# Kernel optimization log

Measured on AMD Instinct MI355X. Metric: run time of the kernel, lower is better.

Reference implementation:

```python
import jax, jax.numpy as jnp
import numpy as np

B, T, D = 8, 4096, 1024

def setup_inputs() -> dict:
    key = jax.random.key(0)
    ks = jax.random.split(key, 7)
    s1 = 1.0 / np.sqrt(D)
    return {
        "x":  jax.random.normal(ks[0], (B, T, D), dtype=jnp.float32),
        "W1": jax.random.normal(ks[1], (D, D), dtype=jnp.float32) * s1,   # attn_1.weight [out,in]
        "b1": jnp.zeros((D,), dtype=jnp.float32),
        "w2": jax.random.normal(ks[2], (1, D), dtype=jnp.float32) * s1,   # attn_2.weight [1,in]
        "b2": jnp.zeros((1,), dtype=jnp.float32),
        "Wc": jax.random.normal(ks[3], (D, 2 * D), dtype=jnp.float32) * (1.0 / np.sqrt(2 * D)),
        "bc": jnp.zeros((D,), dtype=jnp.float32),
    }

def reference(x, W1, b1, w2, b2, Wc, bc):
    # additive attention scores: [B, T, 1] -> [B, T]
    h = jnp.tanh(jnp.einsum('btd,ed->bte', x, W1) + b1)
    s = (jnp.einsum('btd,od->bto', h, w2) + b2)[..., 0]          # [B, T]
    # causal prefix softmax via cumulative sums (single O(T) pass).
    # softmax is shift-invariant, so subtracting the global per-batch max is stable.
    m = jnp.max(s, axis=1, keepdims=True)                        # [B, 1]
    e = jnp.exp(s - m)                                           # [B, T]
    num = jnp.cumsum(e[..., None] * x, axis=1)                   # [B, T, D]
    den = jnp.cumsum(e, axis=1)[..., None]                       # [B, T, 1]
    ctx = num / den                                              # [B, T, D]
    combined = jnp.concatenate((ctx, x), axis=2)                 # [B, T, 2D]
    out = jnp.tanh(jnp.einsum('btk,dk->btd', combined, Wc) + bc)
    return out
```

## Files before the change

kernel.cpp:

```cpp
#include <hip/hip_runtime.h>
#include <cmath>


#define Mtot 32768
#define Dd 1024
#define Tt 4096
#define Bb 8
#define NCHUNK 64
#define TCH 64

typedef __bf16 bf16x8 __attribute__((ext_vector_type(8)));
typedef float f32x4 __attribute__((ext_vector_type(4)));

__device__ __forceinline__ unsigned short f2bf(float f) {
  unsigned int u = __float_as_uint(f);
  unsigned int r = (u + 0x7FFFu + ((u >> 16) & 1u)) >> 16;
  return (unsigned short)r;
}
__device__ __forceinline__ float bf2f(unsigned short s) {
  return __uint_as_float(((unsigned int)s) << 16);
}
__device__ __forceinline__ float tanh_fast(float x) {
  return 1.0f - __fdividef(2.0f, __expf(2.0f * x) + 1.0f);
}

__device__ __forceinline__ void gload16(const unsigned short* g, unsigned short* l) {
  __builtin_amdgcn_global_load_lds(
      (const __attribute__((address_space(1))) unsigned int*)g,
      (__attribute__((address_space(3))) unsigned int*)l, 16, 0, 0);
}

__device__ __forceinline__ void mfma_core256(
    const unsigned short* __restrict__ A0, const unsigned short* __restrict__ A1,
    const unsigned short* __restrict__ W, int ldw, int Ktot,
    int m0, int n0, unsigned short* lds, f32x4 acc[8][4]) {
  const int tid = threadIdx.x;
  const int lane = tid & 63, w = tid >> 6;
  const int wm = w >> 2, wn = w & 3;
  const int quad = lane >> 4, c = lane & 15;
  const int lrow = lane >> 3;
  const int col8 = (lane & 7) ^ lrow;
  const int NK = Ktot >> 6;

#define STG(dst, kt_) do {                                                        \
    int k0_ = (kt_) << 6;                                                         \
    const unsigned short* Asrc_ = (k0_ < 1024) ? A0 : A1;                         \
    int ka_ = k0_ & 1023;                                                         \
    _Pragma("unroll")                                                             \
    for (int j = 0; j < 4; ++j) {                                                 \
      int rb_ = j * 64 + w * 8;                                                   \
      gload16(Asrc_ + (size_t)(m0 + rb_ + lrow) * 1024 + ka_ + col8 * 8,          \
              (dst) + rb_ * 64);                                                  \
      gload16(W + (size_t)(n0 + rb_ + lrow) * ldw + k0_ + col8 * 8,               \
              (dst) + 16384 + rb_ * 64);                                          \
    }                                                                             \
  } while (0)

  STG(lds, 0);

#pragma unroll 1
  for (int kt = 0; kt < NK; ++kt) {
    unsigned short* cur = lds + (kt & 1) * 32768;
    unsigned short* nxt = lds + ((kt + 1) & 1) * 32768;
    if (kt + 1 < NK) {
      STG(nxt, kt + 1);
      asm volatile("s_waitcnt vmcnt(8)" ::: "memory");
    } else {
      asm volatile("s_waitcnt vmcnt(0)" ::: "memory");
    }
    __builtin_amdgcn_s_barrier();
    asm volatile("" ::: "memory");

    const unsigned short* As = cur;
    const unsigned short* Bs = cur + 16384;
    bf16x8 bfr[4];
#pragma unroll
    for (int p = 0; p < 4; ++p) {
      const int ks = p >> 1, mh = p & 1;
      if (mh == 0) {
#pragma unroll
        for (int jn = 0; jn < 4; ++jn) {
          int rb = wn * 64 + jn * 16 + c;
          int pb = (ks * 4 + quad) ^ (rb & 7);
          bfr[jn] = *(const bf16x8*)(Bs + rb * 64 + pb * 8);
        }
      }
      bf16x8 af[4];
#pragma unroll
      for (int ii = 0; ii < 4; ++ii) {
        int ra = wm * 128 + (mh * 4 + ii) * 16 + c;
        int pa = (ks * 4 + quad) ^ (ra & 7);
        af[ii] = *(const bf16x8*)(As + ra * 64 + pa * 8);
      }
      asm volatile("" ::: "memory");
      __builtin_amdgcn_s_barrier();
      asm volatile("s_waitcnt lgkmcnt(0)" ::: "memory");
      __builtin_amdgcn_sched_barrier(0);
      __builtin_amdgcn_s_setprio(1);
#pragma unroll
      for (int ii = 0; ii < 4; ++ii)
#pragma unroll
        for (int jn = 0; jn < 4; ++jn)
          acc[mh * 4 + ii][jn] = __builtin_amdgcn_mfma_f32_16x16x32_bf16(
              af[ii], bfr[jn], acc[mh * 4 + ii][jn], 0, 0, 0);
      __builtin_amdgcn_s_setprio(0);
      asm volatile("" ::: "memory");
      __builtin_amdgcn_s_barrier();
      asm volatile("" ::: "memory");
    }
  }
#undef STG
}

__global__ __launch_bounds__(512, 2) void gemm_s(
    const unsigned short* __restrict__ xb, const unsigned short* __restrict__ W1b,
    const float* __restrict__ b1, const float* __restrict__ w2, float* __restrict__ s) {
  __shared__ __align__(16) unsigned short lds[65536];
  f32x4 acc[8][4];
#pragma unroll
  for (int i = 0; i < 8; ++i)
#pragma unroll
    for (int j = 0; j < 4; ++j) acc[i][j] = (f32x4){0.f, 0.f, 0.f, 0.f};
  int bid = blockIdx.x;
  int swz = (bid & 7) * 64 + (bid >> 3);
  int m0 = (swz >> 2) * 256, n0 = (swz & 3) * 256;
  mfma_core256(xb, xb, W1b, 1024, 1024, m0, n0, lds, acc);
  int tid = threadIdx.x, lane = tid & 63, w = tid >> 6;
  int wm = w >> 2, wn = w & 3, quad = lane >> 4, c = lane & 15;
  float w2v[4], b1v[4];
#pragma unroll
  for (int jn = 0; jn < 4; ++jn) {
    int n = n0 + wn * 64 + jn * 16 + c;
    w2v[jn] = w2[n];
    b1v[jn] = b1[n];
  }
#pragma unroll
  for (int i = 0; i < 8; ++i) {
#pragma unroll
    for (int r = 0; r < 4; ++r) {
      float p = 0.f;
#pragma unroll
      for (int jn = 0; jn < 4; ++jn) p += w2v[jn] * tanh_fast(acc[i][jn][r] + b1v[jn]);
      p += __shfl_xor(p, 1, 64);
      p += __shfl_xor(p, 2, 64);
      p += __shfl_xor(p, 4, 64);
      p += __shfl_xor(p, 8, 64);
      if (c == 0) atomicAdd(&s[m0 + wm * 128 + i * 16 + quad * 4 + r], p);
    }
  }
}

__global__ __launch_bounds__(512, 2) void gemm_out(
    const unsigned short* __restrict__ qb, const unsigned short* __restrict__ xb,
    const unsigned short* __restrict__ Wcb, const float* __restrict__ bc_,
    float* __restrict__ out) {
  __shared__ __align__(16) unsigned short lds[65536];
  f32x4 acc[8][4];
#pragma unroll
  for (int i = 0; i < 8; ++i)
#pragma unroll
    for (int j = 0; j < 4; ++j) acc[i][j] = (f32x4){0.f, 0.f, 0.f, 0.f};
  int bid = blockIdx.x;
  int swz = (bid & 7) * 64 + (bid >> 3);
  int m0 = (swz >> 2) * 256, n0 = (swz & 3) * 256;
  mfma_core256(qb, xb, Wcb, 2048, 2048, m0, n0, lds, acc);
  int tid = threadIdx.x, lane = tid & 63, w = tid >> 6;
  int wm = w >> 2, wn = w & 3, quad = lane >> 4, c = lane & 15;
#pragma unroll
  for (int jn = 0; jn < 4; ++jn) {
    int n = n0 + wn * 64 + jn * 16 + c;
    float bias = bc_[n];
#pragma unroll
    for (int i = 0; i < 8; ++i) {
#pragma unroll
      for (int r = 0; r < 4; ++r) {
        int m = m0 + wm * 128 + i * 16 + quad * 4 + r;
        out[(size_t)m * Dd + n] = tanh_fast(acc[i][jn][r] + bias);
      }
    }
  }
}

__global__ __launch_bounds__(256) void cast_all(
    const float4* __restrict__ x, const float4* __restrict__ W1,
    const float4* __restrict__ Wc, ushort4* __restrict__ xb,
    ushort4* __restrict__ W1b, ushort4* __restrict__ Wcb,
    float4* __restrict__ s) {
  int i = blockIdx.x * 256 + threadIdx.x;
  if (i < 8388608) {
    float4 v = x[i];
    ushort4 o;
    o.x = f2bf(v.x); o.y = f2bf(v.y); o.z = f2bf(v.z); o.w = f2bf(v.w);
    xb[i] = o;
  } else if (i < 8650752) {
    int p = i - 8388608;
    float4 v = W1[p];
    ushort4 o;
    o.x = f2bf(v.x); o.y = f2bf(v.y); o.z = f2bf(v.z); o.w = f2bf(v.w);
    W1b[p] = o;
  } else if (i < 9175040) {
    int p = i - 8650752;
    float4 v = Wc[p];
    ushort4 o;
    o.x = f2bf(v.x); o.y = f2bf(v.y); o.z = f2bf(v.z); o.w = f2bf(v.w);
    Wcb[p] = o;
  } else {
    s[i - 9175040] = (float4){0.f, 0.f, 0.f, 0.f};
  }
}

__global__ __launch_bounds__(256) void softmax_scan(
    const float* __restrict__ s, float* __restrict__ e, float* __restrict__ den) {
  int b = blockIdx.x, tid = threadIdx.x;
  int lane = tid & 63, wid = tid >> 6;
  __shared__ float redm[4], wsum[4];
  const float4* sb4 = (const float4*)(s + (size_t)b * Tt);
  float v[16];
#pragma unroll
  for (int j = 0; j < 4; ++j) {
    float4 f = sb4[tid * 4 + j];
    v[j * 4 + 0] = f.x; v[j * 4 + 1] = f.y; v[j * 4 + 2] = f.z; v[j * 4 + 3] = f.w;
  }
  float m = v[0];
#pragma unroll
  for (int j = 1; j < 16; ++j) m = fmaxf(m, v[j]);
#pragma unroll
  for (int off = 32; off > 0; off >>= 1) m = fmaxf(m, __shfl_xor(m, off, 64));
  if (lane == 0) redm[wid] = m;
  __syncthreads();
  m = fmaxf(fmaxf(redm[0], redm[1]), fmaxf(redm[2], redm[3]));
  float ev[16];
  float ls = 0.f;
#pragma unroll
  for (int j = 0; j < 16; ++j) { ev[j] = __expf(v[j] - m); ls += ev[j]; }
  float sc = ls;
#pragma unroll
  for (int off = 1; off < 64; off <<= 1) {
    float tt = __shfl_up(sc, off, 64);
    if (lane >= off) sc += tt;
  }
  if (lane == 63) wsum[wid] = sc;
  __syncthreads();
  float woff = 0.f;
#pragma unroll
  for (int w = 0; w < 4; ++w) woff += (w < wid) ? wsum[w] : 0.f;
  float run = sc - ls + woff;
  float4* eb4 = (float4*)(e + (size_t)b * Tt);
  float4* db4 = (float4*)(den + (size_t)b * Tt);
#pragma unroll
  for (int j = 0; j < 4; ++j) {
    float4 eo, doo;
    run += ev[j * 4 + 0]; eo.x = ev[j * 4 + 0]; doo.x = run;
    run += ev[j * 4 + 1]; eo.y = ev[j * 4 + 1]; doo.y = run;
    run += ev[j * 4 + 2]; eo.z = ev[j * 4 + 2]; doo.z = run;
    run += ev[j * 4 + 3]; eo.w = ev[j * 4 + 3]; doo.w = run;
    eb4[tid * 4 + j] = eo;
    db4[tid * 4 + j] = doo;
  }
}

__global__ __launch_bounds__(1024) void chunk_sums(
    const unsigned short* __restrict__ xb, const float* __restrict__ e,
    float* __restrict__ S) {
  int bc = blockIdx.x;
  int b = bc >> 6, c = bc & 63;
  int d = threadIdx.x;
  const unsigned short* xp = xb + ((size_t)(b * Tt + c * TCH)) * Dd + d;
  const float* eb = e + (size_t)b * Tt + c * TCH;
  float acc = 0.f;
#pragma unroll 8
  for (int t = 0; t < TCH; ++t) acc += eb[t] * bf2f(xp[(size_t)t * Dd]);
  S[((size_t)bc) * Dd + d] = acc;
}

__global__ __launch_bounds__(256) void chunk_prefix(float* __restrict__ S) {
  int idx = blockIdx.x * 256 + threadIdx.x;
  int b = idx >> 10, d = idx & 1023;
  float* Sb = S + (size_t)b * NCHUNK * Dd + d;
  float acc = 0.f;
#pragma unroll 8
  for (int c = 0; c < NCHUNK; ++c) {
    float t = Sb[(size_t)c * Dd];
    Sb[(size_t)c * Dd] = acc;
    acc += t;
  }
}

__global__ __launch_bounds__(1024) void scan_q(
    const unsigned short* __restrict__ xb, const float* __restrict__ e,
    const float* __restrict__ den, const float* __restrict__ S,
    unsigned short* __restrict__ qb) {
  int bc = blockIdx.x;
  int b = bc >> 6, c = bc & 63;
  int d = threadIdx.x;
  int tbase = b * Tt + c * TCH;
  float acc = S[((size_t)bc) * Dd + d];
  const unsigned short* xp = xb + (size_t)tbase * Dd + d;
  const float* eb = e + tbase;
  const float* db = den + tbase;
  unsigned short* qp = qb + (size_t)tbase * Dd + d;
#pragma unroll 4
  for (int t = 0; t < TCH; ++t) {
    acc += eb[t] * bf2f(xp[(size_t)t * Dd]);
    qp[(size_t)t * Dd] = f2bf(acc * __fdividef(1.0f, db[t]));
  }
}

extern "C" void kernel_launch(void* const* d_in, const int* in_sizes, int n_in,
                              void* d_out, int out_size, void* d_ws, size_t ws_size,
                              hipStream_t stream) {
  const float* x  = (const float*)d_in[0];
  const float* W1 = (const float*)d_in[1];
  const float* b1 = (const float*)d_in[2];
  const float* w2 = (const float*)d_in[3];
  const float* Wc = (const float*)d_in[5];
  const float* bc = (const float*)d_in[6];
  float* out = (float*)d_out;

  float* ws = (float*)d_ws;
  float* s_buf   = ws;
  float* e_buf   = ws + 32768;
  float* den_buf = ws + 65536;
  float* S_buf   = ws + 98304;
  unsigned short* qb  = (unsigned short*)(ws + 622592);
  unsigned short* xb  = (unsigned short*)(ws + 17399808);
  unsigned short* W1b = (unsigned short*)(ws + 34177024);
  unsigned short* Wcb = (unsigned short*)(ws + 34701312);

  cast_all<<<35872, 256, 0, stream>>>((const float4*)x, (const float4*)W1,
                                      (const float4*)Wc, (ushort4*)xb,
                                      (ushort4*)W1b, (ushort4*)Wcb,
                                      (float4*)s_buf);

  gemm_s<<<512, 512, 0, stream>>>(xb, W1b, b1, w2, s_buf);
  softmax_scan<<<Bb, 256, 0, stream>>>(s_buf, e_buf, den_buf);
  chunk_sums<<<Bb * NCHUNK, 1024, 0, stream>>>(xb, e_buf, S_buf);
  chunk_prefix<<<Bb * Dd / 256, 256, 0, stream>>>(S_buf);
  scan_q<<<Bb * NCHUNK, 1024, 0, stream>>>(xb, e_buf, den_buf, S_buf, qb);
  gemm_out<<<512, 512, 0, stream>>>(qb, xb, Wcb, bc, out);
}
```

Measured before the change: 496.3 us.

## Split GEMM k-tile staging into half-k sub-tiles interleaved with MFMA phases

Reorganizes the LDS layout of each 64-wide k tile into two 32-wide halves with a 4-way XOR swizzle. Global-to-LDS loads for the next tile are spread across the four MFMA phases instead of being issued all at once at the top of the iteration. Finer-grained vmcnt waits let compute on the first half proceed while the second half is still loading. The aim is to hide load latency and drop one barrier per iteration. The cost is more complex wait bookkeeping and a risk of races if the vmcnt counts are wrong.

New measurement: 501.8 us. Within noise of the previous version (+1.1%).

```diff
diff --git a/kernel.cpp b/kernel.cpp
--- a/kernel.cpp
+++ b/kernel.cpp
@@ -38,41 +38,38 @@
   const int lane = tid & 63, w = tid >> 6;
   const int wm = w >> 2, wn = w & 3;
   const int quad = lane >> 4, c = lane & 15;
-  const int lrow = lane >> 3;
-  const int col8 = (lane & 7) ^ lrow;
+  const int lr16 = lane >> 2;
+  const int csw = (lane & 3) ^ (lr16 & 3);
   const int NK = Ktot >> 6;
 
-#define STG(dst, kt_) do {                                                        \
-    int k0_ = (kt_) << 6;                                                         \
+#define STGA(dstbase, kt_, h_) do {                                               \
+    int k0_ = ((kt_) << 6) + (h_) * 32;                                           \
     const unsigned short* Asrc_ = (k0_ < 1024) ? A0 : A1;                         \
     int ka_ = k0_ & 1023;                                                         \
     _Pragma("unroll")                                                             \
-    for (int j = 0; j < 4; ++j) {                                                 \
-      int rb_ = j * 64 + w * 8;                                                   \
-      gload16(Asrc_ + (size_t)(m0 + rb_ + lrow) * 1024 + ka_ + col8 * 8,          \
-              (dst) + rb_ * 64);                                                  \
-      gload16(W + (size_t)(n0 + rb_ + lrow) * ldw + k0_ + col8 * 8,               \
-              (dst) + 16384 + rb_ * 64);                                          \
+    for (int j = 0; j < 2; ++j) {                                                 \
+      gload16(Asrc_ + (size_t)(m0 + j * 128 + w * 16 + lr16) * 1024 + ka_ + csw * 8, \
+              (dstbase) + (h_) * 8192 + (j * 128 + w * 16) * 32);                 \
     }                                                                             \
   } while (0)
-
-  STG(lds, 0);
+#define STGB(dstbase, kt_, h_) do {                                               \
+    int k0_ = ((kt_) << 6) + (h_) * 32;                                           \
+    _Pragma("unroll")                                                             \
+    for (int j = 0; j < 2; ++j) {                                                 \
+      gload16(W + (size_t)(n0 + j * 128 + w * 16 + lr16) * ldw + k0_ + csw * 8,   \
+              (dstbase) + 16384 + (h_) * 8192 + (j * 128 + w * 16) * 32);         \
+    }                                                                             \
+  } while (0)
+
+  STGA(lds, 0, 0); STGB(lds, 0, 0); STGA(lds, 0, 1); STGB(lds, 0, 1);
+  asm volatile("s_waitcnt vmcnt(4)" ::: "memory");
+  __builtin_amdgcn_s_barrier();
 
 #pragma unroll 1
   for (int kt = 0; kt < NK; ++kt) {
     unsigned short* cur = lds + (kt & 1) * 32768;
     unsigned short* nxt = lds + ((kt + 1) & 1) * 32768;
-    if (kt + 1 < NK) {
-      STG(nxt, kt + 1);
-      asm volatile("s_waitcnt vmcnt(8)" ::: "memory");
-    } else {
-      asm volatile("s_waitcnt vmcnt(0)" ::: "memory");
-    }
-    __builtin_amdgcn_s_barrier();
-    asm volatile("" ::: "memory");
-
-    const unsigned short* As = cur;
-    const unsigned short* Bs = cur + 16384;
+    const bool more = (kt + 1 < NK);
     bf16x8 bfr[4];
 #pragma unroll
     for (int p = 0; p < 4; ++p) {
@@ -81,16 +78,25 @@
 #pragma unroll
         for (int jn = 0; jn < 4; ++jn) {
           int rb = wn * 64 + jn * 16 + c;
-          int pb = (ks * 4 + quad) ^ (rb & 7);
-          bfr[jn] = *(const bf16x8*)(Bs + rb * 64 + pb * 8);
+          bfr[jn] = *(const bf16x8*)(cur + 16384 + ks * 8192 + rb * 32 +
+                                     ((quad ^ (c & 3)) * 8));
         }
       }
       bf16x8 af[4];
 #pragma unroll
       for (int ii = 0; ii < 4; ++ii) {
         int ra = wm * 128 + (mh * 4 + ii) * 16 + c;
-        int pa = (ks * 4 + quad) ^ (ra & 7);
-        af[ii] = *(const bf16x8*)(As + ra * 64 + pa * 8);
+        af[ii] = *(const bf16x8*)(cur + ks * 8192 + ra * 32 + ((quad ^ (c & 3)) * 8));
+      }
+      if (more) {
+        if (p == 0) STGA(nxt, kt + 1, 0);
+        else if (p == 1) STGB(nxt, kt + 1, 0);
+        else if (p == 2) STGA(nxt, kt + 1, 1);
+        else STGB(nxt, kt + 1, 1);
+      }
+      if (p == 1) {
+        if (more) asm volatile("s_waitcnt vmcnt(4)" ::: "memory");
+        else      asm volatile("s_waitcnt vmcnt(0)" ::: "memory");
       }
       asm volatile("" ::: "memory");
       __builtin_amdgcn_s_barrier();
@@ -104,12 +110,13 @@
           acc[mh * 4 + ii][jn] = __builtin_amdgcn_mfma_f32_16x16x32_bf16(
               af[ii], bfr[jn], acc[mh * 4 + ii][jn], 0, 0, 0);
       __builtin_amdgcn_s_setprio(0);
+      if (p == 3 && more) asm volatile("s_waitcnt vmcnt(4)" ::: "memory");
       asm volatile("" ::: "memory");
       __builtin_amdgcn_s_barrier();
-      asm volatile("" ::: "memory");
     }
   }
-#undef STG
+#undef STGA
+#undef STGB
 }
 
 __global__ __launch_bounds__(512, 2) void gemm_s(
```
